# Kernel optimization log

Hardware: AMD Instinct MI355X
Metric: run time of the kernel (lower is better)

## Reference

```python
import jax, jax.numpy as jnp
import numpy as np

SIGMA_SPATIAL = 1.0
SIGMA_BILATERAL = 0.25
RADIUS = 1
PATCH = 2 * RADIUS + 1  # 3


def _spatial_kernel():
    x, y = np.mgrid[-RADIUS:RADIUS + 1, -RADIUS:RADIUS + 1]
    w1 = np.exp(-(x ** 2 + y ** 2) / (2.0 * SIGMA_SPATIAL ** 2))
    return jnp.asarray(w1.reshape(-1), dtype=jnp.float32)  # [PATCH*PATCH]


def _extract_patches(x):
    # x: [B,H,W,C] -> [B,H,W,PATCH*PATCH,C] via reflect-padded shifted slices
    B, H, W, C = x.shape
    xp = jnp.pad(x, ((0, 0), (RADIUS, RADIUS), (RADIUS, RADIUS), (0, 0)), mode='reflect')
    return jnp.stack(
        [xp[:, dy:dy + H, dx:dx + W, :] for dy in range(PATCH) for dx in range(PATCH)],
        axis=3,
    )


def setup_inputs() -> dict:
    key = jax.random.key(0)
    k1, k2 = jax.random.split(key)
    src = jax.random.uniform(k1, (2, 512, 512, 21), dtype=jnp.float32)
    im = jax.random.uniform(k2, (2, 512, 512, 3), dtype=jnp.float32)
    return {"src": src, "im": im}


def reference(src, im):
    w1 = _spatial_kernel()  # [9]
    im_patches = _extract_patches(im)                      # [B,H,W,9,Ci]
    diff2 = jnp.sum((im_patches - im[:, :, :, None, :]) ** 2, axis=-1)  # [B,H,W,9]
    w = jnp.exp(-diff2 / (2.0 * SIGMA_BILATERAL ** 2)) * w1            # [B,H,W,9]
    src_patches = _extract_patches(src)                    # [B,H,W,9,Cs]
    num = jnp.sum(src_patches * w[..., None], axis=3)      # [B,H,W,Cs]
    den = jnp.sum(w, axis=3, keepdims=True)                # [B,H,W,1]
    return num / den
```

## Files before the change

kernel.cpp:

```cpp
#include <hip/hip_runtime.h>

#define BATCH 2
#define H 512
#define W 512
#define CS 21
#define CI 3
#define P 128
#define R 4
#define TPB 256
#define GROWS (R + 2)
#define GSL (P + 2)
#define GSZ (GROWS * GSL * CI)

__device__ __forceinline__ void fma4(float4& a, const float4 v, const float w) {
    a.x = fmaf(v.x, w, a.x);
    a.y = fmaf(v.y, w, a.y);
    a.z = fmaf(v.z, w, a.z);
    a.w = fmaf(v.w, w, a.w);
}

__global__ __launch_bounds__(TPB, 4) void jbu_kernel(
    const float* __restrict__ src, const float* __restrict__ im,
    float* __restrict__ out)
{
    __shared__ float s_g[GSZ];
    __shared__ __align__(16) float s_w[R * P * 12];

    const int t = threadIdx.x;

    const int f      = blockIdx.x;
    const int xcd    = f & 7;
    const int g      = f >> 3;
    const int rowgrp = (xcd << 4) | (g & 15);
    const int rem    = g >> 4;
    const int x0     = (rem & 3) << 7;
    const int b      = rem >> 2;
    const int y0     = rowgrp << 2;

    int ty[GROWS];
    #pragma unroll
    for (int rr = 0; rr < GROWS; ++rr) {
        int v = y0 - 1 + rr;
        ty[rr] = (v < 0) ? 1 : ((v >= H) ? 2 * H - 2 - v : v);
    }

    const float* imb = im + (size_t)b * (H * W * CI);
    for (int i = t; i < GSZ; i += TPB) {
        int rr   = i / (GSL * CI);
        int remi = i - rr * (GSL * CI);
        int slot = remi / CI;
        int ch   = remi - slot * CI;
        int gx   = x0 + slot - 1;
        gx = (gx < 0) ? 1 : ((gx >= W) ? W - 2 : gx);
        s_g[i] = imb[(ty[rr] * W + gx) * CI + ch];
    }
    __syncthreads();

    {
        const float w1k[9] = {0.36787944f, 0.60653066f, 0.36787944f,
                              0.60653066f, 1.0f,        0.60653066f,
                              0.36787944f, 0.60653066f, 0.36787944f};
        #pragma unroll
        for (int ii = 0; ii < (R * P) / TPB; ++ii) {
            int idx = ii * TPB + t;
            int r   = idx >> 7;
            int px  = idx & (P - 1);
            int cb  = ((r + 1) * GSL + px + 1) * CI;
            float c0 = s_g[cb + 0], c1 = s_g[cb + 1], c2 = s_g[cb + 2];
            float wv[9];
            float den = 0.f;
            #pragma unroll
            for (int k = 0; k < 9; ++k) {
                int dy = k / 3, dx = k % 3;
                int ib = ((r + dy) * GSL + px + dx) * CI;
                float d0 = s_g[ib + 0] - c0;
                float d1 = s_g[ib + 1] - c1;
                float d2 = s_g[ib + 2] - c2;
                float w = __expf(-8.0f * (d0 * d0 + d1 * d1 + d2 * d2)) * w1k[k];
                wv[k] = w;
                den += w;
            }
            float inv = 1.0f / den;
            float* wd = &s_w[idx * 12];
            *(float4*)(wd + 0) = make_float4(wv[0] * inv, wv[1] * inv, wv[2] * inv, wv[3] * inv);
            *(float4*)(wd + 4) = make_float4(wv[4] * inv, wv[5] * inv, wv[6] * inv, wv[7] * inv);
            wd[8] = wv[8] * inv;
        }
    }
    __syncthreads();

    const size_t rs = (size_t)W * CS;
    const float* sb = src + (size_t)b * H * rs;
    const float* srow[GROWS];
    #pragma unroll
    for (int rr = 0; rr < GROWS; ++rr)
        srow[rr] = sb + (size_t)ty[rr] * rs + (size_t)x0 * CS;
    float* ob = out + ((size_t)(b * H + y0)) * rs + (size_t)x0 * CS;

    #pragma unroll
    for (int it = 0; it < (P * 6) / TPB; ++it) {
        int item = it * TPB + t;
        int px = item / 6;
        int q  = item - px * 6;
        int coff = (q == 5) ? 17 : (q << 2);
        int x  = x0 + px;
        int xm = (x == 0)     ? 1     : x - 1;
        int xp = (x == W - 1) ? W - 2 : x + 1;
        int om = (xm - x0) * CS + coff;
        int oc = px * CS + coff;
        int op = (xp - x0) * CS + coff;

        float4 v[GROWS][3];
        #pragma unroll
        for (int rr = 0; rr < GROWS; ++rr) {
            v[rr][0] = *(const float4*)(srow[rr] + om);
            v[rr][1] = *(const float4*)(srow[rr] + oc);
            v[rr][2] = *(const float4*)(srow[rr] + op);
        }

        #pragma unroll
        for (int j = 0; j < R; ++j) {
            const float* wd = &s_w[(((j << 7) + px)) * 12];
            float4 wA = *(const float4*)(wd + 0);
            float4 wB = *(const float4*)(wd + 4);
            float  w8 = wd[8];
            float4 acc = {0.f, 0.f, 0.f, 0.f};
            fma4(acc, v[j + 0][0], wA.x);
            fma4(acc, v[j + 0][1], wA.y);
            fma4(acc, v[j + 0][2], wA.z);
            fma4(acc, v[j + 1][0], wA.w);
            fma4(acc, v[j + 1][1], wB.x);
            fma4(acc, v[j + 1][2], wB.y);
            fma4(acc, v[j + 2][0], wB.z);
            fma4(acc, v[j + 2][1], wB.w);
            fma4(acc, v[j + 2][2], w8);
            *(float4*)(ob + (size_t)j * rs + oc) = acc;
        }
    }
}

extern "C" void kernel_launch(void* const* d_in, const int* in_sizes, int n_in,
                              void* d_out, int out_size, void* d_ws, size_t ws_size,
                              hipStream_t stream) {
    const float* src = (const float*)d_in[0];
    const float* im  = (const float*)d_in[1];
    float* out = (float*)d_out;
    dim3 grid((W / P) * (H / R) * BATCH, 1, 1);
    jbu_kernel<<<grid, TPB, 0, stream>>>(src, im, out);
}
```

Baseline: 105.8 us.

## Prefetch src rows before weight phase, async LDS guide loads, nontemporal stores

Issues the first iteration's src loads for four rows into registers before the guide-image staging and weight computation, so global latency overlaps with the LDS weight phase. Guide-image staging now uses global_load_lds to copy straight into shared memory without passing through registers. Output stores become nontemporal to avoid cache pollution. The prefetched registers raise register pressure, which could reduce occupancy under the 4-block launch bound.

```diff
diff --git a/kernel.cpp b/kernel.cpp
--- a/kernel.cpp
+++ b/kernel.cpp
@@ -11,12 +11,19 @@
 #define GROWS (R + 2)
 #define GSL (P + 2)
 #define GSZ (GROWS * GSL * CI)
+#define PRE_ROWS 4
+
+typedef float f32x4 __attribute__((ext_vector_type(4)));
 
 __device__ __forceinline__ void fma4(float4& a, const float4 v, const float w) {
     a.x = fmaf(v.x, w, a.x);
     a.y = fmaf(v.y, w, a.y);
     a.z = fmaf(v.z, w, a.z);
     a.w = fmaf(v.w, w, a.w);
+}
+
+__device__ __forceinline__ void nt_store4(float* p, const float4 v) {
+    __builtin_nontemporal_store(*(const f32x4*)&v, (f32x4*)p);
 }
 
 __global__ __launch_bounds__(TPB, 4) void jbu_kernel(
@@ -37,11 +44,32 @@
     const int b      = rem >> 2;
     const int y0     = rowgrp << 2;
 
-    int ty[GROWS];
+    const size_t rs = (size_t)W * CS;
+    const float* sb = src + (size_t)b * H * rs;
+    const float* srow[GROWS];
     #pragma unroll
     for (int rr = 0; rr < GROWS; ++rr) {
         int v = y0 - 1 + rr;
-        ty[rr] = (v < 0) ? 1 : ((v >= H) ? 2 * H - 2 - v : v);
+        int tyr = (v < 0) ? 1 : ((v >= H) ? 2 * H - 2 - v : v);
+        srow[rr] = sb + (size_t)tyr * rs + (size_t)x0 * CS;
+    }
+
+    const int px0   = t / 6;
+    const int q0    = t - px0 * 6;
+    const int coff0 = (q0 == 5) ? 17 : (q0 << 2);
+    const int x_    = x0 + px0;
+    const int xm_   = (x_ == 0)     ? 1     : x_ - 1;
+    const int xp_   = (x_ == W - 1) ? W - 2 : x_ + 1;
+    const int om0   = (xm_ - x0) * CS + coff0;
+    const int oc0   = px0 * CS + coff0;
+    const int op0   = (xp_ - x0) * CS + coff0;
+
+    float4 v0[PRE_ROWS][3];
+    #pragma unroll
+    for (int rr = 0; rr < PRE_ROWS; ++rr) {
+        v0[rr][0] = *(const float4*)(srow[rr] + om0);
+        v0[rr][1] = *(const float4*)(srow[rr] + oc0);
+        v0[rr][2] = *(const float4*)(srow[rr] + op0);
     }
 
     const float* imb = im + (size_t)b * (H * W * CI);
@@ -52,7 +80,12 @@
         int ch   = remi - slot * CI;
         int gx   = x0 + slot - 1;
         gx = (gx < 0) ? 1 : ((gx >= W) ? W - 2 : gx);
-        s_g[i] = imb[(ty[rr] * W + gx) * CI + ch];
+        int vv = y0 - 1 + rr;
+        int tyr = (vv < 0) ? 1 : ((vv >= H) ? 2 * H - 2 - vv : vv);
+        const float* gsrc = imb + ((size_t)tyr * W + gx) * CI + ch;
+        __builtin_amdgcn_global_load_lds(
+            (const __attribute__((address_space(1))) void*)gsrc,
+            (__attribute__((address_space(3))) void*)(s_g + i), 4, 0, 0);
     }
     __syncthreads();
 
@@ -89,16 +122,42 @@
     }
     __syncthreads();
 
-    const size_t rs = (size_t)W * CS;
-    const float* sb = src + (size_t)b * H * rs;
-    const float* srow[GROWS];
+    float* ob = out + ((size_t)(b * H + y0)) * rs + (size_t)x0 * CS;
+
+    {
+        float4 v[GROWS][3];
+        #pragma unroll
+        for (int rr = 0; rr < PRE_ROWS; ++rr) {
+            v[rr][0] = v0[rr][0]; v[rr][1] = v0[rr][1]; v[rr][2] = v0[rr][2];
+        }
+        #pragma unroll
+        for (int rr = PRE_ROWS; rr < GROWS; ++rr) {
+            v[rr][0] = *(const float4*)(srow[rr] + om0);
+            v[rr][1] = *(const float4*)(srow[rr] + oc0);
+            v[rr][2] = *(const float4*)(srow[rr] + op0);
+        }
+        #pragma unroll
+        for (int j = 0; j < R; ++j) {
+            const float* wd = &s_w[(((j << 7) + px0)) * 12];
+            float4 wA = *(const float4*)(wd + 0);
+            float4 wB = *(const float4*)(wd + 4);
+            float  w8 = wd[8];
+            float4 acc = {0.f, 0.f, 0.f, 0.f};
+            fma4(acc, v[j + 0][0], wA.x);
+            fma4(acc, v[j + 0][1], wA.y);
+            fma4(acc, v[j + 0][2], wA.z);
+            fma4(acc, v[j + 1][0], wA.w);
+            fma4(acc, v[j + 1][1], wB.x);
+            fma4(acc, v[j + 1][2], wB.y);
+            fma4(acc, v[j + 2][0], wB.z);
+            fma4(acc, v[j + 2][1], wB.w);
+            fma4(acc, v[j + 2][2], w8);
+            nt_store4(ob + (size_t)j * rs + oc0, acc);
+        }
+    }
+
     #pragma unroll
-    for (int rr = 0; rr < GROWS; ++rr)
-        srow[rr] = sb + (size_t)ty[rr] * rs + (size_t)x0 * CS;
-    float* ob = out + ((size_t)(b * H + y0)) * rs + (size_t)x0 * CS;
-
-    #pragma unroll
-    for (int it = 0; it < (P * 6) / TPB; ++it) {
+    for (int it = 1; it < (P * 6) / TPB; ++it) {
         int item = it * TPB + t;
         int px = item / 6;
         int q  = item - px * 6;
@@ -134,7 +193,7 @@
             fma4(acc, v[j + 2][0], wB.z);
             fma4(acc, v[j + 2][1], wB.w);
             fma4(acc, v[j + 2][2], w8);
-            *(float4*)(ob + (size_t)j * rs + oc) = acc;
+            nt_store4(ob + (size_t)j * rs + oc, acc);
         }
     }
 }
```

After: 102.7 us. -2.9%, faster.

## Double rows per block, prefetch src before weight phase, use async LDS loads

Applied to the files above, without the earlier changes.

Raises the rows per block from 4 to 8, so each src row fetched is reused by more outputs and the halo fraction drops. Src loads for the first work items are issued before the guide-image staging and weight computation, so global latency overlaps that phase. The guide is staged with global_load_lds direct-to-LDS loads, and outputs use nontemporal stores. This costs more registers and lowers occupancy (launch bounds 2), and halves the grid.

```diff
diff --git a/kernel.cpp b/kernel.cpp
--- a/kernel.cpp
+++ b/kernel.cpp
@@ -6,11 +6,13 @@
 #define CS 21
 #define CI 3
 #define P 128
-#define R 4
+#define R 8
 #define TPB 256
 #define GROWS (R + 2)
 #define GSL (P + 2)
 #define GSZ (GROWS * GSL * CI)
+
+typedef float f32x4 __attribute__((ext_vector_type(4)));
 
 __device__ __forceinline__ void fma4(float4& a, const float4 v, const float w) {
     a.x = fmaf(v.x, w, a.x);
@@ -19,7 +21,42 @@
     a.w = fmaf(v.w, w, a.w);
 }
 
-__global__ __launch_bounds__(TPB, 4) void jbu_kernel(
+__device__ __forceinline__ void nt_store4(float* p, const float4 v) {
+    __builtin_nontemporal_store(*(const f32x4*)&v, (f32x4*)p);
+}
+
+#define LOAD3(dst, rr, om, oc, op)                              \
+    (dst)[0] = *(const float4*)(srow[rr] + (om));               \
+    (dst)[1] = *(const float4*)(srow[rr] + (oc));               \
+    (dst)[2] = *(const float4*)(srow[rr] + (op));
+
+#define VA_I(r) ((r) < 6 ? (r) : 5)
+#define VB_I(r) ((r) < 6 ? 0 : (r) - 6)
+#define VR(va, vb, r, k) ((r) < 6 ? (va)[VA_I(r)][(k)] : (vb)[VB_I(r)][(k)])
+
+#define COMPUTE8(va, vb, px, oc)                                             \
+    {                                                                        \
+        _Pragma("unroll")                                                    \
+        for (int j = 0; j < R; ++j) {                                        \
+            const float* wd = &s_w[((j << 7) + (px)) * 12];                  \
+            float4 wA = *(const float4*)(wd + 0);                            \
+            float4 wB = *(const float4*)(wd + 4);                            \
+            float  w8 = wd[8];                                               \
+            float4 acc = {0.f, 0.f, 0.f, 0.f};                               \
+            fma4(acc, VR(va, vb, j + 0, 0), wA.x);                           \
+            fma4(acc, VR(va, vb, j + 0, 1), wA.y);                           \
+            fma4(acc, VR(va, vb, j + 0, 2), wA.z);                           \
+            fma4(acc, VR(va, vb, j + 1, 0), wA.w);                           \
+            fma4(acc, VR(va, vb, j + 1, 1), wB.x);                           \
+            fma4(acc, VR(va, vb, j + 1, 2), wB.y);                           \
+            fma4(acc, VR(va, vb, j + 2, 0), wB.z);                           \
+            fma4(acc, VR(va, vb, j + 2, 1), wB.w);                           \
+            fma4(acc, VR(va, vb, j + 2, 2), w8);                             \
+            nt_store4(ob + (size_t)j * rs + (oc), acc);                      \
+        }                                                                    \
+    }
+
+__global__ __launch_bounds__(TPB, 2) void jbu_kernel(
     const float* __restrict__ src, const float* __restrict__ im,
     float* __restrict__ out)
 {
@@ -31,18 +68,35 @@
     const int f      = blockIdx.x;
     const int xcd    = f & 7;
     const int g      = f >> 3;
-    const int rowgrp = (xcd << 4) | (g & 15);
-    const int rem    = g >> 4;
+    const int rowgrp = (xcd << 3) | (g & 7);
+    const int rem    = g >> 3;
     const int x0     = (rem & 3) << 7;
     const int b      = rem >> 2;
-    const int y0     = rowgrp << 2;
-
-    int ty[GROWS];
+    const int y0     = rowgrp << 3;
+
+    const size_t rs = (size_t)W * CS;
+    const float* sb = src + (size_t)b * H * rs;
+    const float* srow[GROWS];
     #pragma unroll
     for (int rr = 0; rr < GROWS; ++rr) {
         int v = y0 - 1 + rr;
-        ty[rr] = (v < 0) ? 1 : ((v >= H) ? 2 * H - 2 - v : v);
-    }
+        int tyr = (v < 0) ? 1 : ((v >= H) ? 2 * H - 2 - v : v);
+        srow[rr] = sb + (size_t)tyr * rs + (size_t)x0 * CS;
+    }
+
+    const int px0   = t / 6;
+    const int q0    = t - px0 * 6;
+    const int coff0 = (q0 == 5) ? 17 : (q0 << 2);
+    const int x_    = x0 + px0;
+    const int xm_   = (x_ == 0)     ? 1     : x_ - 1;
+    const int xp_   = (x_ == W - 1) ? W - 2 : x_ + 1;
+    const int om0   = (xm_ - x0) * CS + coff0;
+    const int oc0   = px0 * CS + coff0;
+    const int op0   = (xp_ - x0) * CS + coff0;
+
+    float4 va0[6][3];
+    #pragma unroll
+    for (int rr = 0; rr < 6; ++rr) { LOAD3(va0[rr], rr, om0, oc0, op0) }
 
     const float* imb = im + (size_t)b * (H * W * CI);
     for (int i = t; i < GSZ; i += TPB) {
@@ -52,9 +106,29 @@
         int ch   = remi - slot * CI;
         int gx   = x0 + slot - 1;
         gx = (gx < 0) ? 1 : ((gx >= W) ? W - 2 : gx);
-        s_g[i] = imb[(ty[rr] * W + gx) * CI + ch];
+        int vv = y0 - 1 + rr;
+        int tyr = (vv < 0) ? 1 : ((vv >= H) ? 2 * H - 2 - vv : vv);
+        const float* gsrc = imb + ((size_t)tyr * W + gx) * CI + ch;
+        __builtin_amdgcn_global_load_lds(
+            (const __attribute__((address_space(1))) void*)gsrc,
+            (__attribute__((address_space(3))) void*)(s_g + i), 4, 0, 0);
     }
     __syncthreads();
+
+    const int item1 = TPB + t;
+    const int px1   = item1 / 6;
+    const int q1    = item1 - px1 * 6;
+    const int coff1 = (q1 == 5) ? 17 : (q1 << 2);
+    const int x1    = x0 + px1;
+    const int xm1   = (x1 == 0)     ? 1     : x1 - 1;
+    const int xp1   = (x1 == W - 1) ? W - 2 : x1 + 1;
+    const int om1   = (xm1 - x0) * CS + coff1;
+    const int oc1   = px1 * CS + coff1;
+    const int op1   = (xp1 - x0) * CS + coff1;
+
+    float4 va1[6][3];
+    #pragma unroll
+    for (int rr = 0; rr < 4; ++rr) { LOAD3(va1[rr], rr, om1, oc1, op1) }
 
     {
         const float w1k[9] = {0.36787944f, 0.60653066f, 0.36787944f,
@@ -89,53 +163,43 @@
     }
     __syncthreads();
 
-    const size_t rs = (size_t)W * CS;
-    const float* sb = src + (size_t)b * H * rs;
-    const float* srow[GROWS];
-    #pragma unroll
-    for (int rr = 0; rr < GROWS; ++rr)
-        srow[rr] = sb + (size_t)ty[rr] * rs + (size_t)x0 * CS;
     float* ob = out + ((size_t)(b * H + y0)) * rs + (size_t)x0 * CS;
 
-    #pragma unroll
-    for (int it = 0; it < (P * 6) / TPB; ++it) {
-        int item = it * TPB + t;
-        int px = item / 6;
-        int q  = item - px * 6;
-        int coff = (q == 5) ? 17 : (q << 2);
-        int x  = x0 + px;
-        int xm = (x == 0)     ? 1     : x - 1;
-        int xp = (x == W - 1) ? W - 2 : x + 1;
-        int om = (xm - x0) * CS + coff;
-        int oc = px * CS + coff;
-        int op = (xp - x0) * CS + coff;
-
-        float4 v[GROWS][3];
-        #pragma unroll
-        for (int rr = 0; rr < GROWS; ++rr) {
-            v[rr][0] = *(const float4*)(srow[rr] + om);
-            v[rr][1] = *(const float4*)(srow[rr] + oc);
-            v[rr][2] = *(const float4*)(srow[rr] + op);
-        }
-
-        #pragma unroll
-        for (int j = 0; j < R; ++j) {
-            const float* wd = &s_w[(((j << 7) + px)) * 12];
-            float4 wA = *(const float4*)(wd + 0);
-            float4 wB = *(const float4*)(wd + 4);
-            float  w8 = wd[8];
-            float4 acc = {0.f, 0.f, 0.f, 0.f};
-            fma4(acc, v[j + 0][0], wA.x);
-            fma4(acc, v[j + 0][1], wA.y);
-            fma4(acc, v[j + 0][2], wA.z);
-            fma4(acc, v[j + 1][0], wA.w);
-            fma4(acc, v[j + 1][1], wB.x);
-            fma4(acc, v[j + 1][2], wB.y);
-            fma4(acc, v[j + 2][0], wB.z);
-            fma4(acc, v[j + 2][1], wB.w);
-            fma4(acc, v[j + 2][2], w8);
-            *(float4*)(ob + (size_t)j * rs + oc) = acc;
-        }
+    {
+        float4 vb0[4][3];
+        #pragma unroll
+        for (int rr = 0; rr < 4; ++rr) { LOAD3(vb0[rr], rr + 6, om0, oc0, op0) }
+        COMPUTE8(va0, vb0, px0, oc0)
+    }
+
+    {
+        LOAD3(va1[4], 4, om1, oc1, op1)
+        LOAD3(va1[5], 5, om1, oc1, op1)
+        float4 vb1[4][3];
+        #pragma unroll
+        for (int rr = 0; rr < 4; ++rr) { LOAD3(vb1[rr], rr + 6, om1, oc1, op1) }
+        COMPUTE8(va1, vb1, px1, oc1)
+    }
+
+    {
+        const int item2 = 2 * TPB + t;
+        const int px2   = item2 / 6;
+        const int q2    = item2 - px2 * 6;
+        const int coff2 = (q2 == 5) ? 17 : (q2 << 2);
+        const int x2    = x0 + px2;
+        const int xm2   = (x2 == 0)     ? 1     : x2 - 1;
+        const int xp2   = (x2 == W - 1) ? W - 2 : x2 + 1;
+        const int om2   = (xm2 - x0) * CS + coff2;
+        const int oc2   = px2 * CS + coff2;
+        const int op2   = (xp2 - x0) * CS + coff2;
+
+        float4 va2[6][3];
+        #pragma unroll
+        for (int rr = 0; rr < 6; ++rr) { LOAD3(va2[rr], rr, om2, oc2, op2) }
+        float4 vb2[4][3];
+        #pragma unroll
+        for (int rr = 0; rr < 4; ++rr) { LOAD3(vb2[rr], rr + 6, om2, oc2, op2) }
+        COMPUTE8(va2, vb2, px2, oc2)
     }
 }
 
```

Result: faster. 101.4 us, median of 2 (-4.1%).

## Drop shared-memory staging; compute weights per thread with rolling row buffer

Applied to the files above, without the earlier changes.

Removes the LDS staging of guide image and precomputed weights along with both __syncthreads. Each thread now loads its guide and source neighbours straight from global memory and recomputes the bilateral weights in registers. It walks 8 rows with a 4-slot rolling register window so each loaded row is reused by three outputs. Tiles shrink to 32 pixels x 8 rows with 192 threads, and output writes become nontemporal stores. In exchange, the weights are recomputed redundantly by the six channel threads of each pixel, and the guide loads become small uncoalesced scalar reads.

```diff
diff --git a/kernel.cpp b/kernel.cpp
--- a/kernel.cpp
+++ b/kernel.cpp
@@ -5,12 +5,12 @@
 #define W 512
 #define CS 21
 #define CI 3
-#define P 128
-#define R 4
-#define TPB 256
+#define P 32
+#define R 8
+#define TPB 192
 #define GROWS (R + 2)
-#define GSL (P + 2)
-#define GSZ (GROWS * GSL * CI)
+
+typedef float f32x4 __attribute__((ext_vector_type(4)));
 
 __device__ __forceinline__ void fma4(float4& a, const float4 v, const float w) {
     a.x = fmaf(v.x, w, a.x);
@@ -19,124 +19,112 @@
     a.w = fmaf(v.w, w, a.w);
 }
 
-__global__ __launch_bounds__(TPB, 4) void jbu_kernel(
+__device__ __forceinline__ void nt_store4(float* p, const float4 v) {
+    __builtin_nontemporal_store(*(const f32x4*)&v, (f32x4*)p);
+}
+
+__device__ __forceinline__ int refl(int v) {
+    return (v < 0) ? 1 : ((v >= H) ? 2 * H - 2 - v : v);
+}
+
+__global__ __launch_bounds__(TPB, 6) void jbu_kernel(
     const float* __restrict__ src, const float* __restrict__ im,
     float* __restrict__ out)
 {
-    __shared__ float s_g[GSZ];
-    __shared__ __align__(16) float s_w[R * P * 12];
-
     const int t = threadIdx.x;
 
     const int f      = blockIdx.x;
     const int xcd    = f & 7;
     const int g      = f >> 3;
-    const int rowgrp = (xcd << 4) | (g & 15);
-    const int rem    = g >> 4;
-    const int x0     = (rem & 3) << 7;
-    const int b      = rem >> 2;
-    const int y0     = rowgrp << 2;
+    const int rowgrp = (xcd << 3) | (g & 7);
+    const int rem    = g >> 3;
+    const int x0     = (rem & 15) << 5;
+    const int b      = rem >> 4;
+    const int y0     = rowgrp << 3;
 
-    int ty[GROWS];
-    #pragma unroll
-    for (int rr = 0; rr < GROWS; ++rr) {
-        int v = y0 - 1 + rr;
-        ty[rr] = (v < 0) ? 1 : ((v >= H) ? 2 * H - 2 - v : v);
+    const int px   = t / 6;
+    const int q    = t - px * 6;
+    const int coff = (q == 5) ? 17 : (q << 2);
+    const int x    = x0 + px;
+    const int xm   = (x == 0)     ? 1     : x - 1;
+    const int xp   = (x == W - 1) ? W - 2 : x + 1;
+
+    const size_t rs  = (size_t)W * CS;
+    const float* sb  = src + (size_t)b * H * rs;
+    const float* imb = im  + (size_t)b * (size_t)(H * W * CI);
+    const int om = xm * CS + coff;
+    const int oc = x  * CS + coff;
+    const int op = xp * CS + coff;
+    const int gm = xm * CI;
+    const int gc = x  * CI;
+    const int gp = xp * CI;
+
+    float* ob = out + ((size_t)(b * H + y0)) * rs;
+
+    float4 s[4][3];
+    float  gg[4][3][3];
+
+    const float w1k[9] = {0.36787944f, 0.60653066f, 0.36787944f,
+                          0.60653066f, 1.0f,        0.60653066f,
+                          0.36787944f, 0.60653066f, 0.36787944f};
+
+#define LOADROW(rr, sl)                                                       \
+    {                                                                         \
+        const int    ry = refl(y0 - 1 + (rr));                                \
+        const float* sr = sb  + (size_t)ry * rs;                              \
+        const float* gr = imb + (size_t)ry * (W * CI);                        \
+        s[sl][0] = *(const float4*)(sr + om);                                 \
+        s[sl][1] = *(const float4*)(sr + oc);                                 \
+        s[sl][2] = *(const float4*)(sr + op);                                 \
+        gg[sl][0][0] = gr[gm]; gg[sl][0][1] = gr[gm + 1]; gg[sl][0][2] = gr[gm + 2]; \
+        gg[sl][1][0] = gr[gc]; gg[sl][1][1] = gr[gc + 1]; gg[sl][1][2] = gr[gc + 2]; \
+        gg[sl][2][0] = gr[gp]; gg[sl][2][1] = gr[gp + 1]; gg[sl][2][2] = gr[gp + 2]; \
     }
 
-    const float* imb = im + (size_t)b * (H * W * CI);
-    for (int i = t; i < GSZ; i += TPB) {
-        int rr   = i / (GSL * CI);
-        int remi = i - rr * (GSL * CI);
-        int slot = remi / CI;
-        int ch   = remi - slot * CI;
-        int gx   = x0 + slot - 1;
-        gx = (gx < 0) ? 1 : ((gx >= W) ? W - 2 : gx);
-        s_g[i] = imb[(ty[rr] * W + gx) * CI + ch];
-    }
-    __syncthreads();
-
-    {
-        const float w1k[9] = {0.36787944f, 0.60653066f, 0.36787944f,
-                              0.60653066f, 1.0f,        0.60653066f,
-                              0.36787944f, 0.60653066f, 0.36787944f};
-        #pragma unroll
-        for (int ii = 0; ii < (R * P) / TPB; ++ii) {
-            int idx = ii * TPB + t;
-            int r   = idx >> 7;
-            int px  = idx & (P - 1);
-            int cb  = ((r + 1) * GSL + px + 1) * CI;
-            float c0 = s_g[cb + 0], c1 = s_g[cb + 1], c2 = s_g[cb + 2];
-            float wv[9];
-            float den = 0.f;
-            #pragma unroll
-            for (int k = 0; k < 9; ++k) {
-                int dy = k / 3, dx = k % 3;
-                int ib = ((r + dy) * GSL + px + dx) * CI;
-                float d0 = s_g[ib + 0] - c0;
-                float d1 = s_g[ib + 1] - c1;
-                float d2 = s_g[ib + 2] - c2;
-                float w = __expf(-8.0f * (d0 * d0 + d1 * d1 + d2 * d2)) * w1k[k];
-                wv[k] = w;
-                den += w;
-            }
-            float inv = 1.0f / den;
-            float* wd = &s_w[idx * 12];
-            *(float4*)(wd + 0) = make_float4(wv[0] * inv, wv[1] * inv, wv[2] * inv, wv[3] * inv);
-            *(float4*)(wd + 4) = make_float4(wv[4] * inv, wv[5] * inv, wv[6] * inv, wv[7] * inv);
-            wd[8] = wv[8] * inv;
-        }
-    }
-    __syncthreads();
-
-    const size_t rs = (size_t)W * CS;
-    const float* sb = src + (size_t)b * H * rs;
-    const float* srow[GROWS];
-    #pragma unroll
-    for (int rr = 0; rr < GROWS; ++rr)
-        srow[rr] = sb + (size_t)ty[rr] * rs + (size_t)x0 * CS;
-    float* ob = out + ((size_t)(b * H + y0)) * rs + (size_t)x0 * CS;
+    LOADROW(0, 0)
+    LOADROW(1, 1)
+    LOADROW(2, 2)
 
     #pragma unroll
-    for (int it = 0; it < (P * 6) / TPB; ++it) {
-        int item = it * TPB + t;
-        int px = item / 6;
-        int q  = item - px * 6;
-        int coff = (q == 5) ? 17 : (q << 2);
-        int x  = x0 + px;
-        int xm = (x == 0)     ? 1     : x - 1;
-        int xp = (x == W - 1) ? W - 2 : x + 1;
-        int om = (xm - x0) * CS + coff;
-        int oc = px * CS + coff;
-        int op = (xp - x0) * CS + coff;
-
-        float4 v[GROWS][3];
-        #pragma unroll
-        for (int rr = 0; rr < GROWS; ++rr) {
-            v[rr][0] = *(const float4*)(srow[rr] + om);
-            v[rr][1] = *(const float4*)(srow[rr] + oc);
-            v[rr][2] = *(const float4*)(srow[rr] + op);
+    for (int j = 0; j < R; ++j) {
+        if (j < R - 1) {
+            const int sl = (j + 3) & 3;
+            LOADROW(j + 3, sl)
         }
 
+        const int s0 = (j + 0) & 3;
+        const int s1 = (j + 1) & 3;
+        const int s2 = (j + 2) & 3;
+
+        const float c0 = gg[s1][1][0];
+        const float c1 = gg[s1][1][1];
+        const float c2 = gg[s1][1][2];
+
+        float wv[9];
+        float den = 0.f;
         #pragma unroll
-        for (int j = 0; j < R; ++j) {
-            const float* wd = &s_w[(((j << 7) + px)) * 12];
-            float4 wA = *(const float4*)(wd + 0);
-            float4 wB = *(const float4*)(wd + 4);
-            float  w8 = wd[8];
-            float4 acc = {0.f, 0.f, 0.f, 0.f};
-            fma4(acc, v[j + 0][0], wA.x);
-            fma4(acc, v[j + 0][1], wA.y);
-            fma4(acc, v[j + 0][2], wA.z);
-            fma4(acc, v[j + 1][0], wA.w);
-            fma4(acc, v[j + 1][1], wB.x);
-            fma4(acc, v[j + 1][2], wB.y);
-            fma4(acc, v[j + 2][0], wB.z);
-            fma4(acc, v[j + 2][1], wB.w);
-            fma4(acc, v[j + 2][2], w8);
-            *(float4*)(ob + (size_t)j * rs + oc) = acc;
+        for (int k = 0; k < 9; ++k) {
+            const int dy = k / 3, dx = k % 3;
+            const int sl = (dy == 0) ? s0 : ((dy == 1) ? s1 : s2);
+            const float d0 = gg[sl][dx][0] - c0;
+            const float d1 = gg[sl][dx][1] - c1;
+            const float d2 = gg[sl][dx][2] - c2;
+            const float w = __expf(-8.0f * (d0 * d0 + d1 * d1 + d2 * d2)) * w1k[k];
+            wv[k] = w;
+            den += w;
         }
+        const float inv = 1.0f / den;
+
+        float4 acc = {0.f, 0.f, 0.f, 0.f};
+        #pragma unroll
+        for (int k = 0; k < 9; ++k) {
+            const int dy = k / 3, dx = k % 3;
+            const int sl = (dy == 0) ? s0 : ((dy == 1) ? s1 : s2);
+            fma4(acc, s[sl][dx], wv[k] * inv);
+        }
+        nt_store4(ob + (size_t)j * rs + oc, acc);
     }
+#undef LOADROW
 }
 
 extern "C" void kernel_launch(void* const* d_in, const int* in_sizes, int n_in,
```

Measured after the change: 115.1 us. 8.8% more time.
